# Performance work log

Hardware: AMD Instinct MI355X
Metric: run time of the kernel (lower is better)

The kernel has to match this reference:

```python
import jax, jax.numpy as jnp
import numpy as np


def setup_inputs() -> dict:
    key = jax.random.key(0)
    ks = jax.random.split(key, 12)
    B, N, M, C = 2, 20000, 4096, 6
    S, K, J = 2, 25, 64          # scales, grid cells (2*2+1)^2, neighbors per cell
    Cin = C + 2                   # xy coords concatenated to features
    Cout = 64
    xyz = jax.random.normal(ks[0], (B, N, 3), dtype=jnp.float32)
    feature = jax.random.normal(ks[1], (B, N, C), dtype=jnp.float32)
    new_xyz = jax.random.normal(ks[2], (B, M, 3), dtype=jnp.float32)
    idx = jax.random.randint(ks[3], (S, B, M, K, J), 0, N, dtype=jnp.int32)
    weight = jax.random.uniform(ks[4], (S, B, M, K, J), dtype=jnp.float32)
    conv_w = jax.random.normal(ks[5], (Cout, Cin, K), dtype=jnp.float32) * 0.05
    conv_b = jnp.zeros((Cout,), dtype=jnp.float32)
    mlp_w0 = jax.random.normal(ks[6], (128, S * Cout), dtype=jnp.float32) * 0.05
    mlp_b0 = jnp.zeros((128,), dtype=jnp.float32)
    mlp_w1 = jax.random.normal(ks[7], (256, 128), dtype=jnp.float32) * 0.05
    mlp_b1 = jnp.zeros((256,), dtype=jnp.float32)
    return {"xyz": xyz, "feature": feature, "new_xyz": new_xyz, "idx": idx,
            "weight": weight, "conv_w": conv_w, "conv_b": conv_b,
            "mlp_w0": mlp_w0, "mlp_b0": mlp_b0, "mlp_w1": mlp_w1, "mlp_b1": mlp_b1}


def reference(xyz, feature, new_xyz, idx, weight, conv_w, conv_b,
              mlp_w0, mlp_b0, mlp_w1, mlp_b1):
    # xyz_feature = cat(xy, feature): (B, N, Cin)
    xf = jnp.concatenate([xyz[:, :, :2], feature], axis=-1)
    center2 = new_xyz[:, :, :2]  # (B, M, 2); remaining channels of center are zero

    def per_scale(idx_s, w_s):
        # idx_s, w_s: (B, M, K, J). Gather neighbor features then bilinear-weight.
        gathered = jax.vmap(lambda f, i: f[i])(xf, idx_s)     # (B, M, K, J, Cin)
        nf = jnp.einsum('bmkj,bmkjc->bmkc', w_s, gathered)    # (B, M, K, Cin)
        nf = nf.at[..., :2].add(-center2[:, :, None, :])      # subtract center (xy only)
        # conv2d with kernel (1, K) over the neighbor axis + ReLU
        out = jnp.einsum('bmkc,ock->bom', nf, conv_w) + conv_b[None, :, None]
        return jax.nn.relu(out)                                # (B, Cout, M)

    outs = [per_scale(idx[s], weight[s]) for s in range(idx.shape[0])]
    x = jnp.concatenate(outs, axis=1)                          # (B, S*Cout, M)
    # SharedMLP: 1x1 convs with ReLU (bn=False)
    x = jax.nn.relu(jnp.einsum('bcm,oc->bom', x, mlp_w0) + mlp_b0[None, :, None])
    x = jax.nn.relu(jnp.einsum('bcm,oc->bom', x, mlp_w1) + mlp_b1[None, :, None])
    result_feature = jnp.transpose(x, (0, 2, 1))               # (B, M, 256)
    return new_xyz, result_feature
```

## Files before the change

### kernel.cpp

```cpp
#include <hip/hip_runtime.h>
#include <hip/hip_bf16.h>

#define B 2
#define N 20000
#define M 4096
#define S 2
#define K 25
#define J 64
#define KJ (K*J)
#define TC 32
#define XP 36

typedef unsigned int u32;

__global__ __launch_bounds__(256) void prep_kernel(
    const float* __restrict__ xyz, const float* __restrict__ feature,
    const float* __restrict__ new_xyz, const float* __restrict__ conv_w,
    const float* __restrict__ w0, const float* __restrict__ w1,
    __hip_bfloat16* __restrict__ xfh, float* __restrict__ conv_wT,
    float* __restrict__ w0T, float* __restrict__ w1T,
    float* __restrict__ out_newxyz) {
    const int T1 = B * N * 8;
    const int T2 = 208 * 64;
    const int T3 = B * M * 3;
    const int T4 = 128 * 128;
    const int T5 = 128 * 256;
    int e = blockIdx.x * blockDim.x + threadIdx.x;
    if (e < T1) {
        int r = e >> 3, t = e & 7;
        float v = (t < 2) ? xyz[r * 3 + t] : feature[r * 6 + (t - 2)];
        xfh[e] = __float2bfloat16(v);
    } else if (e < T1 + T2) {
        int e2 = e - T1;
        int i = e2 >> 6, o = e2 & 63;
        conv_wT[e2] = (i < 200) ? conv_w[o * 200 + (i & 7) * 25 + (i >> 3)] : 0.f;
    } else if (e < T1 + T2 + T3) {
        int e3 = e - T1 - T2;
        out_newxyz[e3] = new_xyz[e3];
    } else if (e < T1 + T2 + T3 + T4) {
        int e4 = e - T1 - T2 - T3;
        int c = e4 >> 7, o = e4 & 127;
        w0T[e4] = w0[o * 128 + c];
    } else if (e < T1 + T2 + T3 + T4 + T5) {
        int e5 = e - T1 - T2 - T3 - T4;
        int c = e5 >> 8, o = e5 & 255;
        w1T[e5] = w1[o * 128 + c];
    }
}

__global__ __launch_bounds__(256) void gather_conv_kernel(
    const int* __restrict__ idx, const float* __restrict__ weight,
    const float* __restrict__ new_xyz, const uint4* __restrict__ xfh,
    const float* __restrict__ conv_wT, const float* __restrict__ conv_b,
    float* __restrict__ xmid) {
    __shared__ float snf[208];
    __shared__ float spart[4][64];

    int g = blockIdx.x;
    int m = g & (M - 1);
    int sb = g >> 12;
    int b = sb & (B - 1);
    int s = sb >> 1;
    int tid = threadIdx.x;

    if (tid >= 200 && tid < 208) snf[tid] = 0.f;

    if (tid < 200) {
        const int4*   gi4 = (const int4*)  (idx    + (size_t)g * KJ);
        const float4* gw4 = (const float4*)(weight + (size_t)g * KJ);
        int4   ia = gi4[tid * 2], ib = gi4[tid * 2 + 1];
        float4 wa = gw4[tid * 2], wb = gw4[tid * 2 + 1];

        const uint4* xfb = xfh + (size_t)b * N;
        float acc[8] = {0.f,0.f,0.f,0.f,0.f,0.f,0.f,0.f};
        int   rows[8] = {ia.x, ia.y, ia.z, ia.w, ib.x, ib.y, ib.z, ib.w};
        float wsv[8]  = {wa.x, wa.y, wa.z, wa.w, wb.x, wb.y, wb.z, wb.w};
        #pragma unroll
        for (int j = 0; j < 8; ++j) {
            uint4 r = xfb[rows[j]];
            float w = wsv[j];
            acc[0] = fmaf(w, __uint_as_float(r.x << 16),          acc[0]);
            acc[1] = fmaf(w, __uint_as_float(r.x & 0xffff0000u),  acc[1]);
            acc[2] = fmaf(w, __uint_as_float(r.y << 16),          acc[2]);
            acc[3] = fmaf(w, __uint_as_float(r.y & 0xffff0000u),  acc[3]);
            acc[4] = fmaf(w, __uint_as_float(r.z << 16),          acc[4]);
            acc[5] = fmaf(w, __uint_as_float(r.z & 0xffff0000u),  acc[5]);
            acc[6] = fmaf(w, __uint_as_float(r.w << 16),          acc[6]);
            acc[7] = fmaf(w, __uint_as_float(r.w & 0xffff0000u),  acc[7]);
        }
        #pragma unroll
        for (int d = 1; d < 8; d <<= 1) {
            #pragma unroll
            for (int c = 0; c < 8; ++c) acc[c] += __shfl_xor(acc[c], d, 64);
        }
        if ((tid & 7) == 0) {
            int kk = tid >> 3;
            float cx = new_xyz[(b * M + m) * 3 + 0];
            float cy = new_xyz[(b * M + m) * 3 + 1];
            acc[0] -= cx; acc[1] -= cy;
            float4* s4 = (float4*)&snf[kk * 8];
            s4[0] = make_float4(acc[0], acc[1], acc[2], acc[3]);
            s4[1] = make_float4(acc[4], acc[5], acc[6], acc[7]);
        }
    }
    __syncthreads();

    int o = tid & 63, p = tid >> 6;
    const float4* snf4 = (const float4*)snf;
    float acc2 = 0.f;
    #pragma unroll
    for (int q = 0; q < 13; ++q) {
        float4 v = snf4[p * 13 + q];
        int i = (p * 13 + q) * 4;
        acc2 = fmaf(v.x, conv_wT[(i + 0) * 64 + o], acc2);
        acc2 = fmaf(v.y, conv_wT[(i + 1) * 64 + o], acc2);
        acc2 = fmaf(v.z, conv_wT[(i + 2) * 64 + o], acc2);
        acc2 = fmaf(v.w, conv_wT[(i + 3) * 64 + o], acc2);
    }
    spart[p][o] = acc2;
    __syncthreads();

    if (tid < 64) {
        float v = spart[0][tid] + spart[1][tid] + spart[2][tid] + spart[3][tid] + conv_b[tid];
        v = fmaxf(v, 0.f);
        xmid[((size_t)(b * M + m)) * 128 + s * 64 + tid] = v;
    }
}

__global__ __launch_bounds__(256) void mlp0_kernel(
    float* __restrict__ xmid,
    const float* __restrict__ w0T, const float* __restrict__ b0) {
    __shared__ float ws[128 * 128];
    __shared__ float xs[128 * XP];

    int tid = threadIdx.x;
    int col0 = blockIdx.x * TC;

    {
        const float4* w4 = (const float4*)w0T;
        float4* ws4 = (float4*)ws;
        #pragma unroll
        for (int i = 0; i < 16; ++i) ws4[tid + 256 * i] = w4[tid + 256 * i];
    }
    {
        const float4* xm4 = (const float4*)(xmid + (size_t)col0 * 128);
        #pragma unroll
        for (int r = tid; r < 32 * TC; r += 256) {
            int lc = r >> 5, c4 = r & 31;
            float4 v = xm4[lc * 32 + c4];
            int c = c4 * 4;
            xs[(c + 0) * XP + lc] = v.x;
            xs[(c + 1) * XP + lc] = v.y;
            xs[(c + 2) * XP + lc] = v.z;
            xs[(c + 3) * XP + lc] = v.w;
        }
    }
    __syncthreads();

    int og = tid >> 3, cg = tid & 7;
    int o0 = og * 4, lc0 = cg * 4;
    float acc[4][4];
    #pragma unroll
    for (int i = 0; i < 4; ++i) {
        float bv = b0[o0 + i];
        #pragma unroll
        for (int u = 0; u < 4; ++u) acc[i][u] = bv;
    }
    for (int c = 0; c < 128; ++c) {
        float4 xv = *(const float4*)&xs[c * XP + lc0];
        float4 wv = *(const float4*)&ws[c * 128 + o0];
        acc[0][0] = fmaf(wv.x, xv.x, acc[0][0]);
        acc[0][1] = fmaf(wv.x, xv.y, acc[0][1]);
        acc[0][2] = fmaf(wv.x, xv.z, acc[0][2]);
        acc[0][3] = fmaf(wv.x, xv.w, acc[0][3]);
        acc[1][0] = fmaf(wv.y, xv.x, acc[1][0]);
        acc[1][1] = fmaf(wv.y, xv.y, acc[1][1]);
        acc[1][2] = fmaf(wv.y, xv.z, acc[1][2]);
        acc[1][3] = fmaf(wv.y, xv.w, acc[1][3]);
        acc[2][0] = fmaf(wv.z, xv.x, acc[2][0]);
        acc[2][1] = fmaf(wv.z, xv.y, acc[2][1]);
        acc[2][2] = fmaf(wv.z, xv.z, acc[2][2]);
        acc[2][3] = fmaf(wv.z, xv.w, acc[2][3]);
        acc[3][0] = fmaf(wv.w, xv.x, acc[3][0]);
        acc[3][1] = fmaf(wv.w, xv.y, acc[3][1]);
        acc[3][2] = fmaf(wv.w, xv.z, acc[3][2]);
        acc[3][3] = fmaf(wv.w, xv.w, acc[3][3]);
    }
    #pragma unroll
    for (int u = 0; u < 4; ++u) {
        float4 v = make_float4(fmaxf(acc[0][u], 0.f), fmaxf(acc[1][u], 0.f),
                               fmaxf(acc[2][u], 0.f), fmaxf(acc[3][u], 0.f));
        *(float4*)&xmid[(size_t)(col0 + lc0 + u) * 128 + o0] = v;
    }
}

__global__ __launch_bounds__(256) void mlp1_kernel(
    const float* __restrict__ xmid,
    const float* __restrict__ w1T, const float* __restrict__ b1,
    float* __restrict__ out_rf) {
    __shared__ float ws[128 * 256];
    __shared__ float xs[128 * XP];

    int tid = threadIdx.x;
    int col0 = blockIdx.x * TC;

    {
        const float4* w4 = (const float4*)w1T;
        float4* ws4 = (float4*)ws;
        #pragma unroll
        for (int i = 0; i < 32; ++i) ws4[tid + 256 * i] = w4[tid + 256 * i];
    }
    {
        const float4* xm4 = (const float4*)(xmid + (size_t)col0 * 128);
        #pragma unroll
        for (int r = tid; r < 32 * TC; r += 256) {
            int lc = r >> 5, c4 = r & 31;
            float4 v = xm4[lc * 32 + c4];
            int c = c4 * 4;
            xs[(c + 0) * XP + lc] = v.x;
            xs[(c + 1) * XP + lc] = v.y;
            xs[(c + 2) * XP + lc] = v.z;
            xs[(c + 3) * XP + lc] = v.w;
        }
    }
    __syncthreads();

    int og = tid >> 2, cg = tid & 3;
    int o0 = og * 4, lc0 = cg * 8;
    float acc[4][8];
    #pragma unroll
    for (int i = 0; i < 4; ++i) {
        float bv = b1[o0 + i];
        #pragma unroll
        for (int u = 0; u < 8; ++u) acc[i][u] = bv;
    }
    for (int c = 0; c < 128; ++c) {
        float4 xa = *(const float4*)&xs[c * XP + lc0];
        float4 xb = *(const float4*)&xs[c * XP + lc0 + 4];
        float4 wv = *(const float4*)&ws[c * 256 + o0];
        float xv[8] = {xa.x, xa.y, xa.z, xa.w, xb.x, xb.y, xb.z, xb.w};
        #pragma unroll
        for (int u = 0; u < 8; ++u) {
            acc[0][u] = fmaf(wv.x, xv[u], acc[0][u]);
            acc[1][u] = fmaf(wv.y, xv[u], acc[1][u]);
            acc[2][u] = fmaf(wv.z, xv[u], acc[2][u]);
            acc[3][u] = fmaf(wv.w, xv[u], acc[3][u]);
        }
    }
    #pragma unroll
    for (int u = 0; u < 8; ++u) {
        float4 v = make_float4(fmaxf(acc[0][u], 0.f), fmaxf(acc[1][u], 0.f),
                               fmaxf(acc[2][u], 0.f), fmaxf(acc[3][u], 0.f));
        *(float4*)&out_rf[(size_t)(col0 + lc0 + u) * 256 + o0] = v;
    }
}

extern "C" void kernel_launch(void* const* d_in, const int* in_sizes, int n_in,
                              void* d_out, int out_size, void* d_ws, size_t ws_size,
                              hipStream_t stream) {
    const float* xyz     = (const float*)d_in[0];
    const float* feature = (const float*)d_in[1];
    const float* new_xyz = (const float*)d_in[2];
    const int*   idx     = (const int*)  d_in[3];
    const float* weight  = (const float*)d_in[4];
    const float* conv_w  = (const float*)d_in[5];
    const float* conv_b  = (const float*)d_in[6];
    const float* mlp_w0  = (const float*)d_in[7];
    const float* mlp_b0  = (const float*)d_in[8];
    const float* mlp_w1  = (const float*)d_in[9];
    const float* mlp_b1  = (const float*)d_in[10];

    float* out    = (float*)d_out;
    float* out_rf = out + (size_t)B * M * 3;

    float* wsf = (float*)d_ws;
    __hip_bfloat16* xfh = (__hip_bfloat16*)wsf;
    float* conv_wT = wsf + 160000;
    float* xmid    = conv_wT + 13312;
    float* w0T     = xmid + 1048576;
    float* w1T     = w0T + 16384;

    {
        int total = 320000 + 13312 + 24576 + 16384 + 32768;
        int blocks = (total + 255) / 256;
        prep_kernel<<<blocks, 256, 0, stream>>>(xyz, feature, new_xyz, conv_w,
                                                mlp_w0, mlp_w1,
                                                xfh, conv_wT, w0T, w1T, out);
    }
    {
        int blocks = S * B * M;
        gather_conv_kernel<<<blocks, 256, 0, stream>>>(idx, weight, new_xyz,
                                                       (const uint4*)xfh,
                                                       conv_wT, conv_b, xmid);
    }
    {
        int blocks = (B * M) / TC;
        mlp0_kernel<<<blocks, 256, 0, stream>>>(xmid, w0T, mlp_b0);
    }
    {
        int blocks = (B * M) / TC;
        mlp1_kernel<<<blocks, 256, 0, stream>>>(xmid, w1T, mlp_b1, out_rf);
    }
}
```

Baseline: 384.6 us.

## Stage point features in LDS chunks for gather, batch 8 centers per block

New measurement: 466.2 us. 1.21x slower.

```diff
diff --git a/kernel.cpp b/kernel.cpp
--- a/kernel.cpp
+++ b/kernel.cpp
@@ -8,10 +8,10 @@
 #define K 25
 #define J 64
 #define KJ (K*J)
+#define GM 8
+#define CHUNK 4096
+#define NCHUNK 5
 #define TC 32
-#define XP 36
-
-typedef unsigned int u32;
 
 __global__ __launch_bounds__(256) void prep_kernel(
     const float* __restrict__ xyz, const float* __restrict__ feature,
@@ -48,82 +48,111 @@
     }
 }
 
-__global__ __launch_bounds__(256) void gather_conv_kernel(
+__global__ __launch_bounds__(256, 2) void gather_conv_kernel(
     const int* __restrict__ idx, const float* __restrict__ weight,
     const float* __restrict__ new_xyz, const uint4* __restrict__ xfh,
     const float* __restrict__ conv_wT, const float* __restrict__ conv_b,
     float* __restrict__ xmid) {
-    __shared__ float snf[208];
-    __shared__ float spart[4][64];
+    __shared__ uint4 chunkbuf[CHUNK];
+    __shared__ float snf[GM][208];
 
     int g = blockIdx.x;
-    int m = g & (M - 1);
-    int sb = g >> 12;
-    int b = sb & (B - 1);
+    int m8 = g & 511;
+    int sb = g >> 9;
+    int b = sb & 1;
     int s = sb >> 1;
+    int m0 = m8 * GM;
     int tid = threadIdx.x;
 
-    if (tid >= 200 && tid < 208) snf[tid] = 0.f;
-
-    if (tid < 200) {
-        const int4*   gi4 = (const int4*)  (idx    + (size_t)g * KJ);
-        const float4* gw4 = (const float4*)(weight + (size_t)g * KJ);
-        int4   ia = gi4[tid * 2], ib = gi4[tid * 2 + 1];
-        float4 wa = gw4[tid * 2], wb = gw4[tid * 2 + 1];
-
-        const uint4* xfb = xfh + (size_t)b * N;
-        float acc[8] = {0.f,0.f,0.f,0.f,0.f,0.f,0.f,0.f};
-        int   rows[8] = {ia.x, ia.y, ia.z, ia.w, ib.x, ib.y, ib.z, ib.w};
-        float wsv[8]  = {wa.x, wa.y, wa.z, wa.w, wb.x, wb.y, wb.z, wb.w};
-        #pragma unroll
-        for (int j = 0; j < 8; ++j) {
-            uint4 r = xfb[rows[j]];
-            float w = wsv[j];
-            acc[0] = fmaf(w, __uint_as_float(r.x << 16),          acc[0]);
-            acc[1] = fmaf(w, __uint_as_float(r.x & 0xffff0000u),  acc[1]);
-            acc[2] = fmaf(w, __uint_as_float(r.y << 16),          acc[2]);
-            acc[3] = fmaf(w, __uint_as_float(r.y & 0xffff0000u),  acc[3]);
-            acc[4] = fmaf(w, __uint_as_float(r.z << 16),          acc[4]);
-            acc[5] = fmaf(w, __uint_as_float(r.z & 0xffff0000u),  acc[5]);
-            acc[6] = fmaf(w, __uint_as_float(r.w << 16),          acc[6]);
-            acc[7] = fmaf(w, __uint_as_float(r.w & 0xffff0000u),  acc[7]);
-        }
-        #pragma unroll
-        for (int d = 1; d < 8; d <<= 1) {
-            #pragma unroll
-            for (int c = 0; c < 8; ++c) acc[c] += __shfl_xor(acc[c], d, 64);
-        }
-        if ((tid & 7) == 0) {
-            int kk = tid >> 3;
-            float cx = new_xyz[(b * M + m) * 3 + 0];
-            float cy = new_xyz[(b * M + m) * 3 + 1];
-            acc[0] -= cx; acc[1] -= cy;
-            float4* s4 = (float4*)&snf[kk * 8];
-            s4[0] = make_float4(acc[0], acc[1], acc[2], acc[3]);
-            s4[1] = make_float4(acc[4], acc[5], acc[6], acc[7]);
-        }
-    }
+    bool active = tid < 200;
+    int mi = tid / 25;
+    int k  = tid - mi * 25;
+
+    int   ir[64];
+    float wr[64];
+    if (active) {
+        size_t base = ((((size_t)(s * B + b)) * M + m0 + mi) * K + k) * J;
+        const int4*   gi4 = (const int4*)  (idx    + base);
+        const float4* gw4 = (const float4*)(weight + base);
+        #pragma unroll
+        for (int q = 0; q < 16; ++q) {
+            int4   iv = gi4[q];
+            float4 wv = gw4[q];
+            ir[q * 4 + 0] = iv.x; ir[q * 4 + 1] = iv.y;
+            ir[q * 4 + 2] = iv.z; ir[q * 4 + 3] = iv.w;
+            wr[q * 4 + 0] = wv.x; wr[q * 4 + 1] = wv.y;
+            wr[q * 4 + 2] = wv.z; wr[q * 4 + 3] = wv.w;
+        }
+    } else {
+        #pragma unroll
+        for (int q = 0; q < 64; ++q) { ir[q] = -1; wr[q] = 0.f; }
+    }
+
+    float acc[8] = {0.f, 0.f, 0.f, 0.f, 0.f, 0.f, 0.f, 0.f};
+
+    const uint4* src = xfh + (size_t)b * N;
+    for (int c = 0; c < NCHUNK; ++c) {
+        int lo = c * CHUNK;
+        int cnt = min(CHUNK, N - lo);
+        __syncthreads();
+        for (int i = tid; i < cnt; i += 256) chunkbuf[i] = src[lo + i];
+        __syncthreads();
+        #pragma unroll
+        for (int p = 0; p < 64; ++p) {
+            unsigned r = (unsigned)(ir[p] - lo);
+            if (r < (unsigned)CHUNK) {
+                uint4 row = chunkbuf[r];
+                float w = wr[p];
+                acc[0] = fmaf(w, __uint_as_float(row.x << 16),         acc[0]);
+                acc[1] = fmaf(w, __uint_as_float(row.x & 0xffff0000u), acc[1]);
+                acc[2] = fmaf(w, __uint_as_float(row.y << 16),         acc[2]);
+                acc[3] = fmaf(w, __uint_as_float(row.y & 0xffff0000u), acc[3]);
+                acc[4] = fmaf(w, __uint_as_float(row.z << 16),         acc[4]);
+                acc[5] = fmaf(w, __uint_as_float(row.z & 0xffff0000u), acc[5]);
+                acc[6] = fmaf(w, __uint_as_float(row.w << 16),         acc[6]);
+                acc[7] = fmaf(w, __uint_as_float(row.w & 0xffff0000u), acc[7]);
+            }
+        }
+    }
+
+    if (active) {
+        float cx = new_xyz[((size_t)b * M + m0 + mi) * 3 + 0];
+        float cy = new_xyz[((size_t)b * M + m0 + mi) * 3 + 1];
+        acc[0] -= cx; acc[1] -= cy;
+        float4* s4 = (float4*)&snf[mi][k * 8];
+        s4[0] = make_float4(acc[0], acc[1], acc[2], acc[3]);
+        s4[1] = make_float4(acc[4], acc[5], acc[6], acc[7]);
+    }
+    if (tid < 64) snf[tid >> 3][200 + (tid & 7)] = 0.f;
     __syncthreads();
 
-    int o = tid & 63, p = tid >> 6;
-    const float4* snf4 = (const float4*)snf;
-    float acc2 = 0.f;
-    #pragma unroll
-    for (int q = 0; q < 13; ++q) {
-        float4 v = snf4[p * 13 + q];
-        int i = (p * 13 + q) * 4;
-        acc2 = fmaf(v.x, conv_wT[(i + 0) * 64 + o], acc2);
-        acc2 = fmaf(v.y, conv_wT[(i + 1) * 64 + o], acc2);
-        acc2 = fmaf(v.z, conv_wT[(i + 2) * 64 + o], acc2);
-        acc2 = fmaf(v.w, conv_wT[(i + 3) * 64 + o], acc2);
-    }
-    spart[p][o] = acc2;
+    {
+        float4* cw4 = (float4*)chunkbuf;
+        const float4* w4 = (const float4*)conv_wT;
+        for (int i = tid; i < 3328; i += 256) cw4[i] = w4[i];
+    }
     __syncthreads();
 
-    if (tid < 64) {
-        float v = spart[0][tid] + spart[1][tid] + spart[2][tid] + spart[3][tid] + conv_b[tid];
-        v = fmaxf(v, 0.f);
-        xmid[((size_t)(b * M + m)) * 128 + s * 64 + tid] = v;
+    {
+        const float* cw = (const float*)chunkbuf;
+        int o = tid & 63, h = tid >> 6;
+        #pragma unroll
+        for (int pass = 0; pass < 2; ++pass) {
+            int mm = pass * 4 + h;
+            float a = conv_b[o];
+            const float4* sm = (const float4*)snf[mm];
+            #pragma unroll 5
+            for (int q = 0; q < 50; ++q) {
+                float4 v = sm[q];
+                int i = q * 4;
+                a = fmaf(v.x, cw[(i + 0) * 64 + o], a);
+                a = fmaf(v.y, cw[(i + 1) * 64 + o], a);
+                a = fmaf(v.z, cw[(i + 2) * 64 + o], a);
+                a = fmaf(v.w, cw[(i + 3) * 64 + o], a);
+            }
+            a = fmaxf(a, 0.f);
+            xmid[((size_t)b * M + m0 + mm) * 128 + s * 64 + o] = a;
+        }
     }
 }
 
@@ -131,7 +160,7 @@
     float* __restrict__ xmid,
     const float* __restrict__ w0T, const float* __restrict__ b0) {
     __shared__ float ws[128 * 128];
-    __shared__ float xs[128 * XP];
+    __shared__ float xs[128 * 32];
 
     int tid = threadIdx.x;
     int col0 = blockIdx.x * TC;
@@ -145,14 +174,14 @@
     {
         const float4* xm4 = (const float4*)(xmid + (size_t)col0 * 128);
         #pragma unroll
-        for (int r = tid; r < 32 * TC; r += 256) {
+        for (int r = tid; r < 1024; r += 256) {
             int lc = r >> 5, c4 = r & 31;
             float4 v = xm4[lc * 32 + c4];
             int c = c4 * 4;
-            xs[(c + 0) * XP + lc] = v.x;
-            xs[(c + 1) * XP + lc] = v.y;
-            xs[(c + 2) * XP + lc] = v.z;
-            xs[(c + 3) * XP + lc] = v.w;
+            xs[(c + 0) * 32 + lc] = v.x;
+            xs[(c + 1) * 32 + lc] = v.y;
+            xs[(c + 2) * 32 + lc] = v.z;
+            xs[(c + 3) * 32 + lc] = v.w;
         }
     }
     __syncthreads();
@@ -167,7 +196,7 @@
         for (int u = 0; u < 4; ++u) acc[i][u] = bv;
     }
     for (int c = 0; c < 128; ++c) {
-        float4 xv = *(const float4*)&xs[c * XP + lc0];
+        float4 xv = *(const float4*)&xs[c * 32 + lc0];
         float4 wv = *(const float4*)&ws[c * 128 + o0];
         acc[0][0] = fmaf(wv.x, xv.x, acc[0][0]);
         acc[0][1] = fmaf(wv.x, xv.y, acc[0][1]);
@@ -198,60 +227,69 @@
     const float* __restrict__ xmid,
     const float* __restrict__ w1T, const float* __restrict__ b1,
     float* __restrict__ out_rf) {
-    __shared__ float ws[128 * 256];
-    __shared__ float xs[128 * XP];
+    __shared__ float ws[128 * 128];
+    __shared__ float xs[128 * 32];
 
     int tid = threadIdx.x;
-    int col0 = blockIdx.x * TC;
-
-    {
-        const float4* w4 = (const float4*)w1T;
-        float4* ws4 = (float4*)ws;
-        #pragma unroll
-        for (int i = 0; i < 32; ++i) ws4[tid + 256 * i] = w4[tid + 256 * i];
+    int bx = blockIdx.x;
+    int col0 = (bx >> 1) * TC;
+    int oH = (bx & 1) * 128;
+
+    {
+        for (int i = tid; i < 4096; i += 256) {
+            int c = i >> 5, q = i & 31;
+            *(float4*)&ws[c * 128 + q * 4] = *(const float4*)&w1T[c * 256 + oH + q * 4];
+        }
     }
     {
         const float4* xm4 = (const float4*)(xmid + (size_t)col0 * 128);
         #pragma unroll
-        for (int r = tid; r < 32 * TC; r += 256) {
+        for (int r = tid; r < 1024; r += 256) {
             int lc = r >> 5, c4 = r & 31;
             float4 v = xm4[lc * 32 + c4];
             int c = c4 * 4;
-            xs[(c + 0) * XP + lc] = v.x;
-            xs[(c + 1) * XP + lc] = v.y;
-            xs[(c + 2) * XP + lc] = v.z;
-            xs[(c + 3) * XP + lc] = v.w;
+            xs[(c + 0) * 32 + lc] = v.x;
+            xs[(c + 1) * 32 + lc] = v.y;
+            xs[(c + 2) * 32 + lc] = v.z;
+            xs[(c + 3) * 32 + lc] = v.w;
         }
     }
     __syncthreads();
 
-    int og = tid >> 2, cg = tid & 3;
-    int o0 = og * 4, lc0 = cg * 8;
-    float acc[4][8];
+    int og = tid >> 3, cg = tid & 7;
+    int o0 = og * 4, lc0 = cg * 4;
+    float acc[4][4];
     #pragma unroll
     for (int i = 0; i < 4; ++i) {
-        float bv = b1[o0 + i];
-        #pragma unroll
-        for (int u = 0; u < 8; ++u) acc[i][u] = bv;
+        float bv = b1[oH + o0 + i];
+        #pragma unroll
+        for (int u = 0; u < 4; ++u) acc[i][u] = bv;
     }
     for (int c = 0; c < 128; ++c) {
-        float4 xa = *(const float4*)&xs[c * XP + lc0];
-        float4 xb = *(const float4*)&xs[c * XP + lc0 + 4];
-        float4 wv = *(const float4*)&ws[c * 256 + o0];
-        float xv[8] = {xa.x, xa.y, xa.z, xa.w, xb.x, xb.y, xb.z, xb.w};
-        #pragma unroll
-        for (int u = 0; u < 8; ++u) {
-            acc[0][u] = fmaf(wv.x, xv[u], acc[0][u]);
-            acc[1][u] = fmaf(wv.y, xv[u], acc[1][u]);
-            acc[2][u] = fmaf(wv.z, xv[u], acc[2][u]);
-            acc[3][u] = fmaf(wv.w, xv[u], acc[3][u]);
-        }
+        float4 xv = *(const float4*)&xs[c * 32 + lc0];
+        float4 wv = *(const float4*)&ws[c * 128 + o0];
+        acc[0][0] = fmaf(wv.x, xv.x, acc[0][0]);
+        acc[0][1] = fmaf(wv.x, xv.y, acc[0][1]);
+        acc[0][2] = fmaf(wv.x, xv.z, acc[0][2]);
+        acc[0][3] = fmaf(wv.x, xv.w, acc[0][3]);
+        acc[1][0] = fmaf(wv.y, xv.x, acc[1][0]);
+        acc[1][1] = fmaf(wv.y, xv.y, acc[1][1]);
+        acc[1][2] = fmaf(wv.y, xv.z, acc[1][2]);
+        acc[1][3] = fmaf(wv.y, xv.w, acc[1][3]);
+        acc[2][0] = fmaf(wv.z, xv.x, acc[2][0]);
+        acc[2][1] = fmaf(wv.z, xv.y, acc[2][1]);
+        acc[2][2] = fmaf(wv.z, xv.z, acc[2][2]);
+        acc[2][3] = fmaf(wv.z, xv.w, acc[2][3]);
+        acc[3][0] = fmaf(wv.w, xv.x, acc[3][0]);
+        acc[3][1] = fmaf(wv.w, xv.y, acc[3][1]);
+        acc[3][2] = fmaf(wv.w, xv.z, acc[3][2]);
+        acc[3][3] = fmaf(wv.w, xv.w, acc[3][3]);
     }
     #pragma unroll
-    for (int u = 0; u < 8; ++u) {
+    for (int u = 0; u < 4; ++u) {
         float4 v = make_float4(fmaxf(acc[0][u], 0.f), fmaxf(acc[1][u], 0.f),
                                fmaxf(acc[2][u], 0.f), fmaxf(acc[3][u], 0.f));
-        *(float4*)&out_rf[(size_t)(col0 + lc0 + u) * 256 + o0] = v;
+        *(float4*)&out_rf[(size_t)(col0 + lc0 + u) * 256 + oH + o0] = v;
     }
 }
 
@@ -288,17 +326,15 @@
                                                 xfh, conv_wT, w0T, w1T, out);
     }
     {
-        int blocks = S * B * M;
+        int blocks = S * B * (M / GM);
         gather_conv_kernel<<<blocks, 256, 0, stream>>>(idx, weight, new_xyz,
                                                        (const uint4*)xfh,
                                                        conv_wT, conv_b, xmid);
     }
     {
-        int blocks = (B * M) / TC;
-        mlp0_kernel<<<blocks, 256, 0, stream>>>(xmid, w0T, mlp_b0);
-    }
-    {
-        int blocks = (B * M) / TC;
-        mlp1_kernel<<<blocks, 256, 0, stream>>>(xmid, w1T, mlp_b1, out_rf);
-    }
-}
+        mlp0_kernel<<<(B * M) / TC, 256, 0, stream>>>(xmid, w0T, mlp_b0);
+    }
+    {
+        mlp1_kernel<<<2 * (B * M) / TC, 256, 0, stream>>>(xmid, w1T, mlp_b1, out_rf);
+    }
+}
```
